# Kernel optimization log

Measured on AMD Instinct MI355X. Metric: run time of the kernel, lower is better.

The kernel has to match this reference:

```python
import jax, jax.numpy as jnp
import numpy as np

DIM = 128
LAYER_GNN = 3
LAYER_CNN = 3
WINDOW = 11
K = 2 * WINDOW + 1  # conv kernel size 23
N_FP = 100000
N_WORD = 10000
N_ATOMS = 8192
L_PROT = 8192


def setup_inputs() -> dict:
    key = jax.random.key(0)
    ks = jax.random.split(key, 12)
    s = 0.1
    # sparse binary molecular adjacency (avg degree ~16), math is still dense matmul
    adjacency = (jax.random.uniform(ks[2], (N_ATOMS, N_ATOMS)) < 0.002).astype(jnp.float32)
    return {
        "fingerprints": jax.random.randint(ks[0], (N_ATOMS,), 0, N_FP),
        "words": jax.random.randint(ks[1], (L_PROT,), 0, N_WORD),
        "adjacency": adjacency,
        "emb_fp": jax.random.normal(ks[3], (N_FP, DIM), jnp.float32) * s,
        "emb_word": jax.random.normal(ks[4], (N_WORD, DIM), jnp.float32) * s,
        "Wg": jax.random.normal(ks[5], (LAYER_GNN, DIM, DIM), jnp.float32) * s,
        "bg": jnp.zeros((LAYER_GNN, DIM), jnp.float32),
        "conv_w": jax.random.normal(ks[6], (LAYER_CNN, 1, 1, K, K), jnp.float32) * s,
        "conv_b": jnp.zeros((LAYER_CNN,), jnp.float32),
        "Wa": jax.random.normal(ks[7], (DIM, DIM), jnp.float32) * s,
        "ba": jnp.zeros((DIM,), jnp.float32),
        "Wo": jax.random.normal(ks[8], (2, 2 * DIM), jnp.float32) * s,
        "bo": jnp.zeros((2,), jnp.float32),
    }


def reference(fingerprints, words, adjacency, emb_fp, emb_word, Wg, bg,
              conv_w, conv_b, Wa, ba, Wo, bo):
    # ---- GNN over compound graph ----
    xs = emb_fp[fingerprints]                      # [N_ATOMS, DIM]
    for i in range(LAYER_GNN):
        hs = jax.nn.relu(xs @ Wg[i].T + bg[i])     # Linear + ReLU
        xs = xs + adjacency @ hs                   # adjacency message passing
    x_compound = jnp.sum(xs, axis=0, keepdims=True)  # [1, DIM]

    # ---- attention-CNN over protein words ----
    xs_p = emb_word[words]                         # [L_PROT, DIM]
    x = x_compound                                 # [1, DIM]
    for i in range(LAYER_CNN):
        img = xs_p[None, None]                     # [1,1,L,DIM]
        h = jax.lax.conv_general_dilated(
            img, conv_w[i], window_strides=(1, 1),
            padding=[(WINDOW, WINDOW), (WINDOW, WINDOW)],
            dimension_numbers=("NCHW", "OIHW", "NCHW"))
        hs = jax.nn.relu(h[0, 0] + conv_b[i])      # [L, DIM]
        x = jax.nn.relu(x @ Wa.T + ba)             # [1, DIM]
        hs = jax.nn.relu(hs @ Wa.T + ba)           # [L, DIM]
        weights = jnp.tanh(x @ hs.T)               # [1, L]
        xs_p = weights.T * hs                      # [L, DIM]
    x_protein = jnp.sum(xs_p, axis=0, keepdims=True)  # [1, DIM]

    y = jnp.concatenate([x_compound, x_protein], axis=1)  # [1, 2*DIM]
    z = jax.nn.softmax(y @ Wo.T + bo, axis=1)
    return z[0]  # [2]
```

## Files before the change

### kernel.cpp

```cpp
#include <hip/hip_runtime.h>
#include <hip/hip_cooperative_groups.h>
#include <math.h>

namespace cg = cooperative_groups;

#define DIM 128
#define NATOMS 8192
#define LPROT 8192
#define CAP 64
#define NF (NATOMS*DIM)
#define NB 256
#define RPB 32
#define TPB 1024


__device__ __forceinline__ void d_ell(int blk, int tid, const float* __restrict__ adj,
                                      int* __restrict__ ell, int* __restrict__ cnt) {
  int wv = tid >> 6, lane = tid & 63;
  for (int rr = 0; rr < 2; ++rr) {
    int row = blk * RPB + wv * 2 + rr;
    const float4* rp = (const float4*)(adj + (size_t)row * NATOMS);
    int* er = ell + (size_t)row * CAP;
    int c = 0;
    for (int it = 0; it < NATOMS / 256; ++it) {
      float4 v = rp[(size_t)it * 64 + lane];
      float f[4] = {v.x, v.y, v.z, v.w};
      #pragma unroll
      for (int j = 0; j < 4; ++j) {
        bool nz = (f[j] != 0.0f);
        unsigned long long m = __ballot(nz);
        if (nz) {
          int pos = c + __popcll(m & ((1ull << lane) - 1ull));
          if (pos < CAP) er[pos] = it * 256 + lane * 4 + j;
        }
        c += __popcll(m);
      }
    }
    if (lane == 0) cnt[row] = c > CAP ? CAP : c;
  }
}

__device__ __forceinline__ void d_stage_w(int tid, const float* __restrict__ WT, float* Ws) {
  for (int i = tid; i < 4096; i += TPB) {
    int r = i >> 5, c = i & 31;
    *(float4*)&Ws[r * 132 + c * 4] = *(const float4*)&WT[r * DIM + c * 4];
  }
}

__device__ __forceinline__ void d_stage_a(int tid, const float* __restrict__ A,
                                          size_t rbase, float* As) {
  for (int i = tid; i < 1024; i += TPB) {
    int r = i >> 5, c = i & 31;
    *(float4*)&As[r * 132 + c * 4] = *(const float4*)&A[(rbase + r) * DIM + c * 4];
  }
}

__device__ __forceinline__ void d_gemm44(int tid, const float* As, const float* Ws,
                                         const float* __restrict__ bias,
                                         float* out, int ostr, size_t obase) {
  if (tid < 256) {
    int j0 = (tid & 31) * 4, r0 = (tid >> 5) * 4;
    float acc[4][4];
    float4 b4 = *(const float4*)&bias[j0];
    #pragma unroll
    for (int ri = 0; ri < 4; ++ri) {
      acc[ri][0] = b4.x; acc[ri][1] = b4.y; acc[ri][2] = b4.z; acc[ri][3] = b4.w;
    }
    for (int k4 = 0; k4 < 32; ++k4) {
      float a[4][4], w[4][4];
      #pragma unroll
      for (int ri = 0; ri < 4; ++ri)
        *(float4*)a[ri] = *(const float4*)&As[(r0 + ri) * 132 + k4 * 4];
      #pragma unroll
      for (int kk = 0; kk < 4; ++kk)
        *(float4*)w[kk] = *(const float4*)&Ws[(k4 * 4 + kk) * 132 + j0];
      #pragma unroll
      for (int ri = 0; ri < 4; ++ri)
        #pragma unroll
        for (int kk = 0; kk < 4; ++kk) {
          acc[ri][0] += a[ri][kk] * w[kk][0];
          acc[ri][1] += a[ri][kk] * w[kk][1];
          acc[ri][2] += a[ri][kk] * w[kk][2];
          acc[ri][3] += a[ri][kk] * w[kk][3];
        }
    }
    #pragma unroll
    for (int ri = 0; ri < 4; ++ri) {
      float4 o;
      o.x = fmaxf(acc[ri][0], 0.f); o.y = fmaxf(acc[ri][1], 0.f);
      o.z = fmaxf(acc[ri][2], 0.f); o.w = fmaxf(acc[ri][3], 0.f);
      *(float4*)&out[(obase + r0 + ri) * (size_t)ostr + j0] = o;
    }
  }
}

__device__ __forceinline__ void d_spmv(int blk, int tid, const int* __restrict__ ell,
                                       const int* __restrict__ cnt,
                                       const float* __restrict__ hs, float* __restrict__ xs) {
  int wv = tid >> 6, lane = tid & 63;
  for (int rr = 0; rr < 2; ++rr) {
    size_t row = (size_t)blk * RPB + wv * 2 + rr;
    int n = cnt[row];
    const int* er = ell + row * CAP;
    float2 a2 = *(const float2*)&xs[row * DIM + lane * 2];
    int t = 0;
    for (; t + 4 <= n; t += 4) {
      int j0 = er[t], j1 = er[t + 1], j2 = er[t + 2], j3 = er[t + 3];
      float2 h0 = *(const float2*)&hs[(size_t)j0 * DIM + lane * 2];
      float2 h1 = *(const float2*)&hs[(size_t)j1 * DIM + lane * 2];
      float2 h2 = *(const float2*)&hs[(size_t)j2 * DIM + lane * 2];
      float2 h3 = *(const float2*)&hs[(size_t)j3 * DIM + lane * 2];
      a2.x += (h0.x + h1.x) + (h2.x + h3.x);
      a2.y += (h0.y + h1.y) + (h2.y + h3.y);
    }
    for (; t < n; ++t) {
      float2 h = *(const float2*)&hs[(size_t)er[t] * DIM + lane * 2];
      a2.x += h.x; a2.y += h.y;
    }
    *(float2*)&xs[row * DIM + lane * 2] = a2;
  }
}

__device__ __forceinline__ void d_colsum(int blk, int tid, const float* __restrict__ src,
                                         float* red, float* __restrict__ dst) {
  int c = tid & 127, h = tid >> 7;
  size_t rbase = (size_t)blk * RPB;
  float s = 0.f;
  for (int r = h; r < RPB; r += 8) s += src[(rbase + r) * DIM + c];
  red[h * DIM + c] = s;
  __syncthreads();
  if (h == 0) {
    float t2 = 0.f;
    #pragma unroll
    for (int w = 0; w < 8; ++w) t2 += red[w * DIM + c];
    atomicAdd(&dst[c], t2);
  }
}

__device__ __forceinline__ void d_xchain(int tid, const float* __restrict__ xc,
                                         const float* __restrict__ WaT,
                                         const float* __restrict__ ba,
                                         float* xb, float* __restrict__ xall) {
  if (tid < DIM) xb[tid] = xc[tid];
  __syncthreads();
  for (int i = 0; i < 3; ++i) {
    float a = 0.f;
    if (tid < DIM) {
      a = ba[tid];
      for (int k = 0; k < DIM; ++k) a += xb[k] * WaT[k * DIM + tid];
      a = fmaxf(a, 0.f);
    }
    __syncthreads();
    if (tid < DIM) { xb[tid] = a; xall[i * DIM + tid] = a; }
    __syncthreads();
  }
}

__device__ __forceinline__ void d_stage_tile(int blk, int tid, const float* __restrict__ cur,
                                             const float* __restrict__ cwl,
                                             float* U, float* wl) {
  for (int i = tid; i < 529; i += TPB) wl[i] = cwl[i];
  int l0 = blk * RPB;
  for (int i = tid; i < 54 * 156; i += TPB) {
    int ll = i / 156, dd = i % 156;
    int gl = l0 - 11 + ll, gd = dd - 11;
    float v = 0.f;
    if (gl >= 0 && gl < LPROT && (unsigned)gd < DIM)
      v = cur[(size_t)gl * DIM + gd];
    U[i] = v;
  }
}

__device__ __forceinline__ void d_conv(int tid, const float* U, const float* wl,
                                       float cbias, float* As) {
  int ro = tid >> 5, d0 = (tid & 31) * 4;
  float acc[4] = {0.f, 0.f, 0.f, 0.f};
  for (int a = 0; a < 23; ++a) {
    float r[26];
    #pragma unroll
    for (int q = 0; q < 6; ++q)
      *(float4*)&r[4 * q] = *(const float4*)&U[(ro + a) * 156 + d0 + 4 * q];
    r[24] = U[(ro + a) * 156 + d0 + 24];
    r[25] = U[(ro + a) * 156 + d0 + 25];
    #pragma unroll
    for (int b = 0; b < 23; ++b) {
      float wb = wl[a * 23 + b];
      #pragma unroll
      for (int m = 0; m < 4; ++m) acc[m] += r[b + m] * wb;
    }
  }
  #pragma unroll
  for (int m = 0; m < 4; ++m)
    As[ro * 132 + d0 + m] = fmaxf(acc[m] + cbias, 0.f);
}

__device__ __forceinline__ void d_attn(int blk, int tid, const float* hs2, const float* xrow,
                                       float* __restrict__ nxt, int last,
                                       float* red, float* __restrict__ xp) {
  int wv = tid >> 6, lane = tid & 63;
  size_t rbase = (size_t)blk * RPB;
  float x0 = xrow[lane * 2], x1 = xrow[lane * 2 + 1];
  float cx = 0.f, cy = 0.f;
  #pragma unroll
  for (int rr = 0; rr < 2; ++rr) {
    int row = wv * 2 + rr;
    float2 h = *(const float2*)&hs2[row * 132 + lane * 2];
    float p = h.x * x0 + h.y * x1;
    #pragma unroll
    for (int s = 32; s > 0; s >>= 1) p += __shfl_xor(p, s, 64);
    float wgt = tanhf(p);
    if (!last) {
      float2 o; o.x = wgt * h.x; o.y = wgt * h.y;
      *(float2*)&nxt[(rbase + row) * DIM + lane * 2] = o;
    } else { cx += wgt * h.x; cy += wgt * h.y; }
  }
  if (last) {
    red[wv * DIM + lane * 2] = cx;
    red[wv * DIM + lane * 2 + 1] = cy;
    __syncthreads();
    if (wv == 0) {
      float sx = 0.f, sy = 0.f;
      #pragma unroll
      for (int w = 0; w < 16; ++w) {
        sx += red[w * DIM + lane * 2];
        sy += red[w * DIM + lane * 2 + 1];
      }
      atomicAdd(&xp[lane * 2], sx);
      atomicAdd(&xp[lane * 2 + 1], sy);
    }
  }
}

__device__ __forceinline__ void d_final(int tid, const float* __restrict__ xc,
                                        const float* __restrict__ xp,
                                        const float* __restrict__ Wo,
                                        const float* __restrict__ bo,
                                        float* fs, float* __restrict__ out) {
  int wv = tid >> 6, lane = tid & 63;
  float p0 = 0.f, p1 = 0.f;
  if (tid < 256) {
    float y = (tid < DIM) ? xc[tid] : xp[tid - DIM];
    p0 = y * Wo[tid];
    p1 = y * Wo[256 + tid];
  }
  #pragma unroll
  for (int s = 32; s > 0; s >>= 1) { p0 += __shfl_xor(p0, s, 64); p1 += __shfl_xor(p1, s, 64); }
  if (tid < 256 && lane == 0) { fs[wv] = p0; fs[16 + wv] = p1; }
  __syncthreads();
  if (tid == 0) {
    float l0 = bo[0], l1 = bo[1];
    #pragma unroll
    for (int w = 0; w < 4; ++w) { l0 += fs[w]; l1 += fs[16 + w]; }
    float m = fmaxf(l0, l1);
    float e0 = expf(l0 - m), e1 = expf(l1 - m);
    out[0] = e0 / (e0 + e1);
    out[1] = e1 / (e0 + e1);
  }
}

__global__ __launch_bounds__(256) void k_prep(
    const int* __restrict__ fp, const int* __restrict__ words,
    const float* __restrict__ emb_fp, const float* __restrict__ emb_w,
    const float* __restrict__ Wg, const float* __restrict__ Wa,
    float* __restrict__ xs, float* __restrict__ xsp,
    float* __restrict__ WgT, float* __restrict__ WaT,
    float* __restrict__ xc, float* __restrict__ xp) {
  int b = blockIdx.x, tid = threadIdx.x;
  if (b < 1024) {
    int i = b * 256 + tid;
    int row = i >> 5, c4 = i & 31;
    ((float4*)(xs + (size_t)row * DIM))[c4] =
        ((const float4*)(emb_fp + (size_t)fp[row] * DIM))[c4];
  } else if (b < 2048) {
    int i = (b - 1024) * 256 + tid;
    int row = i >> 5, c4 = i & 31;
    ((float4*)(xsp + (size_t)row * DIM))[c4] =
        ((const float4*)(emb_w + (size_t)words[row] * DIM))[c4];
  } else if (b < 2112) {
    __shared__ float tile[32][33];
    int sub = b - 2048;
    int m = sub >> 4, t = sub & 15;
    int tx = t & 3, ty = t >> 2;
    const float* src = (m < 3) ? Wg + m * DIM * DIM : Wa;
    float*       dst = (m < 3) ? WgT + m * DIM * DIM : WaT;
    int x = tid & 31, y0 = tid >> 5;
    int xg = tx * 32 + x;
    for (int i = y0; i < 32; i += 8)
      tile[i][x] = src[(ty * 32 + i) * DIM + xg];
    __syncthreads();
    int xo = ty * 32 + x;
    for (int i = y0; i < 32; i += 8)
      dst[(tx * 32 + i) * DIM + xo] = tile[x][i];
  } else {
    if (tid < DIM) { xc[tid] = 0.f; xp[tid] = 0.f; }
  }
}

__global__ __launch_bounds__(TPB, 4) void kg(
    const float* __restrict__ adj, const float* __restrict__ WgT,
    const float* __restrict__ bg, const float* __restrict__ WaT,
    const float* __restrict__ ba, int* __restrict__ ell, int* __restrict__ cnt,
    float* __restrict__ xs, float* __restrict__ hsbA, float* __restrict__ hsbB,
    float* __restrict__ xc, float* __restrict__ xall) {
  cg::grid_group grid = cg::this_grid();
  __shared__ float Ws[128 * 132];
  __shared__ float As[32 * 132];
  __shared__ float red[8 * DIM];
  int tid = threadIdx.x, blk = blockIdx.x;
  size_t rbase = (size_t)blk * RPB;

  d_ell(blk, tid, adj, ell, cnt);
  __syncthreads();
  for (int layer = 0; layer < 3; ++layer) {
    float* hout = (layer == 1) ? hsbB : hsbA;
    d_stage_w(tid, WgT + (size_t)layer * DIM * DIM, Ws);
    d_stage_a(tid, xs, rbase, As);
    __syncthreads();
    d_gemm44(tid, As, Ws, bg + layer * DIM, hout, DIM, rbase);
    grid.sync();
    d_spmv(blk, tid, ell, cnt, hout, xs);
    __syncthreads();
  }
  d_colsum(blk, tid, xs, red, xc);
  grid.sync();
  if (blk == 0) d_xchain(tid, xc, WaT, ba, red, xall);
}

__global__ __launch_bounds__(TPB, 4) void kp(
    const float* __restrict__ cw, const float* __restrict__ cb,
    const float* __restrict__ WaT, const float* __restrict__ ba,
    const float* __restrict__ xall, const float* __restrict__ xc,
    const float* __restrict__ Wo, const float* __restrict__ bo,
    float* __restrict__ bufA, float* __restrict__ bufB,
    float* __restrict__ xp, float* __restrict__ out) {
  cg::grid_group grid = cg::this_grid();
  __shared__ float U[128 * 132];
  __shared__ float wl[529];
  __shared__ float As[32 * 132];
  __shared__ float hs2[32 * 132];
  __shared__ float xrow[DIM];
  __shared__ float fs[32];
  int tid = threadIdx.x, blk = blockIdx.x;

  const float* cur = bufA;
  float* nxt = bufB;
  for (int layer = 0; layer < 3; ++layer) {
    d_stage_tile(blk, tid, cur, cw + layer * 529, U, wl);
    if (tid < DIM) xrow[tid] = xall[layer * DIM + tid];
    __syncthreads();
    d_conv(tid, U, wl, cb[layer], As);
    __syncthreads();
    d_stage_w(tid, WaT, U);
    __syncthreads();
    d_gemm44(tid, As, U, ba, hs2, 132, 0);
    __syncthreads();
    d_attn(blk, tid, hs2, xrow, nxt, layer == 2, As, xp);
    grid.sync();
    const float* t = cur; cur = nxt; nxt = (float*)t;
  }
  if (blk == 0) d_final(tid, xc, xp, Wo, bo, fs, out);
}

__global__ __launch_bounds__(TPB, 4) void fb_ell(const float* __restrict__ adj,
                                                 int* __restrict__ ell, int* __restrict__ cnt) {
  d_ell(blockIdx.x, threadIdx.x, adj, ell, cnt);
}
__global__ __launch_bounds__(TPB, 4) void fb_ggemm(const float* __restrict__ WT,
                                                   const float* __restrict__ bias,
                                                   const float* __restrict__ xs,
                                                   float* __restrict__ hout) {
  __shared__ float Ws[128 * 132];
  __shared__ float As[32 * 132];
  int tid = threadIdx.x;
  size_t rbase = (size_t)blockIdx.x * RPB;
  d_stage_w(tid, WT, Ws);
  d_stage_a(tid, xs, rbase, As);
  __syncthreads();
  d_gemm44(tid, As, Ws, bias, hout, DIM, rbase);
}
__global__ __launch_bounds__(TPB, 4) void fb_spmv(const int* __restrict__ ell,
                                                  const int* __restrict__ cnt,
                                                  const float* __restrict__ hs,
                                                  float* __restrict__ xs) {
  d_spmv(blockIdx.x, threadIdx.x, ell, cnt, hs, xs);
}
__global__ __launch_bounds__(TPB, 4) void fb_colxc(const float* __restrict__ xs,
                                                   float* __restrict__ xc) {
  __shared__ float red[8 * DIM];
  d_colsum(blockIdx.x, threadIdx.x, xs, red, xc);
}
__global__ void fb_xchain(const float* __restrict__ xc, const float* __restrict__ WaT,
                          const float* __restrict__ ba, float* __restrict__ xall) {
  __shared__ float xb[DIM];
  d_xchain(threadIdx.x, xc, WaT, ba, xb, xall);
}
__global__ __launch_bounds__(TPB, 4) void fb_prot(const float* __restrict__ cur,
    float* __restrict__ nxt, const float* __restrict__ cwl, const float* __restrict__ cbp,
    const float* __restrict__ WaT, const float* __restrict__ ba,
    const float* __restrict__ xrow_g, float* __restrict__ xp, int last) {
  __shared__ float U[128 * 132];
  __shared__ float wl[529];
  __shared__ float As[32 * 132];
  __shared__ float hs2[32 * 132];
  __shared__ float xrow[DIM];
  int tid = threadIdx.x, blk = blockIdx.x;
  d_stage_tile(blk, tid, cur, cwl, U, wl);
  if (tid < DIM) xrow[tid] = xrow_g[tid];
  __syncthreads();
  d_conv(tid, U, wl, cbp[0], As);
  __syncthreads();
  d_stage_w(tid, WaT, U);
  __syncthreads();
  d_gemm44(tid, As, U, ba, hs2, 132, 0);
  __syncthreads();
  d_attn(blk, tid, hs2, xrow, nxt, last, As, xp);
}
__global__ void fb_final(const float* __restrict__ xc, const float* __restrict__ xp,
                         const float* __restrict__ Wo, const float* __restrict__ bo,
                         float* __restrict__ out) {
  __shared__ float fs[32];
  d_final(threadIdx.x, xc, xp, Wo, bo, fs, out);
}

extern "C" void kernel_launch(void* const* d_in, const int* in_sizes, int n_in,
                              void* d_out, int out_size, void* d_ws, size_t ws_size,
                              hipStream_t stream) {
  const int*   fp     = (const int*)d_in[0];
  const int*   words  = (const int*)d_in[1];
  const float* adj    = (const float*)d_in[2];
  const float* emb_fp = (const float*)d_in[3];
  const float* emb_w  = (const float*)d_in[4];
  const float* Wg     = (const float*)d_in[5];
  const float* bg     = (const float*)d_in[6];
  const float* cw     = (const float*)d_in[7];
  const float* cb     = (const float*)d_in[8];
  const float* Wa     = (const float*)d_in[9];
  const float* ba     = (const float*)d_in[10];
  const float* Wo     = (const float*)d_in[11];
  const float* bo     = (const float*)d_in[12];
  float* out = (float*)d_out;

  float* ws   = (float*)d_ws;
  float* xs   = ws;
  float* hsbA = ws + (size_t)NF;
  float* hsbB = ws + 2 * (size_t)NF;
  float* bufA = ws + 3 * (size_t)NF;
  int*   ell  = (int*)(ws + 4 * (size_t)NF);
  int*   cnt  = ell + (size_t)NATOMS * CAP;
  float* xc   = (float*)(cnt + NATOMS);
  float* xp   = xc + DIM;
  float* xall = xp + DIM;
  float* WgT  = xall + 3 * DIM;
  float* WaT  = WgT + 3 * DIM * DIM;
  float* bufB = hsbA;

  k_prep<<<dim3(2113), 256, 0, stream>>>(fp, words, emb_fp, emb_w, Wg, Wa,
                                         xs, bufA, WgT, WaT, xc, xp);

  int mg = 0, mp = 0;
  hipError_t e1 = hipOccupancyMaxActiveBlocksPerMultiprocessor(
      &mg, reinterpret_cast<const void*>(kg), TPB, 0);
  hipError_t e2 = hipOccupancyMaxActiveBlocksPerMultiprocessor(
      &mp, reinterpret_cast<const void*>(kp), TPB, 0);
  bool coop = (e1 == hipSuccess && e2 == hipSuccess && mg >= 1 && mp >= 1);

  if (coop) {
    void* ag[] = {(void*)&adj, (void*)&WgT, (void*)&bg, (void*)&WaT, (void*)&ba,
                  (void*)&ell, (void*)&cnt, (void*)&xs, (void*)&hsbA, (void*)&hsbB,
                  (void*)&xc, (void*)&xall};
    if (hipLaunchCooperativeKernel((void*)kg, dim3(NB), dim3(TPB), ag, 0, stream)
        != hipSuccess) {
      coop = false;
    } else {
      void* ap[] = {(void*)&cw, (void*)&cb, (void*)&WaT, (void*)&ba, (void*)&xall,
                    (void*)&xc, (void*)&Wo, (void*)&bo, (void*)&bufA, (void*)&bufB,
                    (void*)&xp, (void*)&out};
      if (hipLaunchCooperativeKernel((void*)kp, dim3(NB), dim3(TPB), ap, 0, stream)
          != hipSuccess)
        coop = false;
    }
  }

  if (!coop) {
    k_prep<<<dim3(2113), 256, 0, stream>>>(fp, words, emb_fp, emb_w, Wg, Wa,
                                           xs, bufA, WgT, WaT, xc, xp);
    fb_ell<<<dim3(NB), TPB, 0, stream>>>(adj, ell, cnt);
    for (int l = 0; l < 3; ++l) {
      float* ho = (l == 1) ? hsbB : hsbA;
      fb_ggemm<<<dim3(NB), TPB, 0, stream>>>(WgT + (size_t)l * DIM * DIM,
                                             bg + l * DIM, xs, ho);
      fb_spmv<<<dim3(NB), TPB, 0, stream>>>(ell, cnt, ho, xs);
    }
    fb_colxc<<<dim3(NB), TPB, 0, stream>>>(xs, xc);
    fb_xchain<<<dim3(1), 128, 0, stream>>>(xc, WaT, ba, xall);
    const float* cur = bufA; float* nxt = bufB;
    for (int l = 0; l < 3; ++l) {
      fb_prot<<<dim3(NB), TPB, 0, stream>>>(cur, nxt, cw + l * 529, cb + l, WaT, ba,
                                            xall + l * DIM, xp, l == 2 ? 1 : 0);
      const float* t = cur; cur = nxt; nxt = (float*)t;
    }
    fb_final<<<dim3(1), 256, 0, stream>>>(xc, xp, Wo, bo, out);
  }
}
```

Baseline: 290.2 us.

## Move ELL construction into prep kernel with prefetching and merge cooperative kernels

The adjacency-to-ELL scan moves out of the cooperative GNN kernel into the wide prep launch, with one wave per row and double-buffered float4 prefetches of eight loads at a time, so the 256MB adjacency read is spread across thousands of blocks instead of 256. The GNN and protein cooperative kernels are merged into one kernel with a grid sync between phases, removing a launch. The merged kernel's shared memory is the union of both kernels' arrays, which may reduce occupancy. The fallback path no longer re-runs prep or ELL building.

```diff
diff --git a/kernel.cpp b/kernel.cpp
--- a/kernel.cpp
+++ b/kernel.cpp
@@ -13,32 +13,6 @@
 #define RPB 32
 #define TPB 1024
 
-
-__device__ __forceinline__ void d_ell(int blk, int tid, const float* __restrict__ adj,
-                                      int* __restrict__ ell, int* __restrict__ cnt) {
-  int wv = tid >> 6, lane = tid & 63;
-  for (int rr = 0; rr < 2; ++rr) {
-    int row = blk * RPB + wv * 2 + rr;
-    const float4* rp = (const float4*)(adj + (size_t)row * NATOMS);
-    int* er = ell + (size_t)row * CAP;
-    int c = 0;
-    for (int it = 0; it < NATOMS / 256; ++it) {
-      float4 v = rp[(size_t)it * 64 + lane];
-      float f[4] = {v.x, v.y, v.z, v.w};
-      #pragma unroll
-      for (int j = 0; j < 4; ++j) {
-        bool nz = (f[j] != 0.0f);
-        unsigned long long m = __ballot(nz);
-        if (nz) {
-          int pos = c + __popcll(m & ((1ull << lane) - 1ull));
-          if (pos < CAP) er[pos] = it * 256 + lane * 4 + j;
-        }
-        c += __popcll(m);
-      }
-    }
-    if (lane == 0) cnt[row] = c > CAP ? CAP : c;
-  }
-}
 
 __device__ __forceinline__ void d_stage_w(int tid, const float* __restrict__ WT, float* Ws) {
   for (int i = tid; i < 4096; i += TPB) {
@@ -258,27 +232,62 @@
   }
 }
 
-__global__ __launch_bounds__(256) void k_prep(
+__global__ __launch_bounds__(256) void k_prep_build(
     const int* __restrict__ fp, const int* __restrict__ words,
     const float* __restrict__ emb_fp, const float* __restrict__ emb_w,
     const float* __restrict__ Wg, const float* __restrict__ Wa,
+    const float* __restrict__ adj,
     float* __restrict__ xs, float* __restrict__ xsp,
     float* __restrict__ WgT, float* __restrict__ WaT,
+    int* __restrict__ ell, int* __restrict__ cnt,
     float* __restrict__ xc, float* __restrict__ xp) {
   int b = blockIdx.x, tid = threadIdx.x;
-  if (b < 1024) {
-    int i = b * 256 + tid;
+  if (b < 2048) {
+    int wv = tid >> 6, lane = tid & 63;
+    int row = b * 4 + wv;
+    const float4* rp = (const float4*)(adj + (size_t)row * NATOMS);
+    int* er = ell + (size_t)row * CAP;
+    int c = 0;
+    float4 buf[8];
+    #pragma unroll
+    for (int u = 0; u < 8; ++u) buf[u] = rp[u * 64 + lane];
+    for (int it = 0; it < 32; it += 8) {
+      float4 nb[8];
+      if (it + 8 < 32) {
+        #pragma unroll
+        for (int u = 0; u < 8; ++u) nb[u] = rp[(it + 8 + u) * 64 + lane];
+      }
+      #pragma unroll
+      for (int u = 0; u < 8; ++u) {
+        float f[4] = {buf[u].x, buf[u].y, buf[u].z, buf[u].w};
+        #pragma unroll
+        for (int j = 0; j < 4; ++j) {
+          bool nz = (f[j] != 0.0f);
+          unsigned long long m = __ballot(nz);
+          if (nz) {
+            int pos = c + __popcll(m & ((1ull << lane) - 1ull));
+            if (pos < CAP) er[pos] = (it + u) * 256 + lane * 4 + j;
+          }
+          c += __popcll(m);
+        }
+      }
+      #pragma unroll
+      for (int u = 0; u < 8; ++u) buf[u] = nb[u];
+    }
+    if (lane == 0) cnt[row] = c > CAP ? CAP : c;
+  } else if (b < 3072) {
+    int i = (b - 2048) * 256 + tid;
     int row = i >> 5, c4 = i & 31;
     ((float4*)(xs + (size_t)row * DIM))[c4] =
         ((const float4*)(emb_fp + (size_t)fp[row] * DIM))[c4];
-  } else if (b < 2048) {
-    int i = (b - 1024) * 256 + tid;
+  } else if (b < 4096) {
+    int i = (b - 3072) * 256 + tid;
     int row = i >> 5, c4 = i & 31;
     ((float4*)(xsp + (size_t)row * DIM))[c4] =
         ((const float4*)(emb_w + (size_t)words[row] * DIM))[c4];
-  } else if (b < 2112) {
+  } else if (b < 4160) {
     __shared__ float tile[32][33];
-    int sub = b - 2048;
+    int sub = b - 4096;
     int m = sub >> 4, t = sub & 15;
     int tx = t & 3, ty = t >> 2;
     const float* src = (m < 3) ? Wg + m * DIM * DIM : Wa;
@@ -296,21 +305,27 @@
   }
 }
 
-__global__ __launch_bounds__(TPB, 4) void kg(
-    const float* __restrict__ adj, const float* __restrict__ WgT,
-    const float* __restrict__ bg, const float* __restrict__ WaT,
-    const float* __restrict__ ba, int* __restrict__ ell, int* __restrict__ cnt,
+__global__ __launch_bounds__(TPB, 4) void kmain(
+    const float* __restrict__ WgT, const float* __restrict__ bg,
+    const float* __restrict__ WaT, const float* __restrict__ ba,
+    const int* __restrict__ ell, const int* __restrict__ cnt,
+    const float* __restrict__ cw, const float* __restrict__ cb,
+    const float* __restrict__ Wo, const float* __restrict__ bo,
     float* __restrict__ xs, float* __restrict__ hsbA, float* __restrict__ hsbB,
-    float* __restrict__ xc, float* __restrict__ xall) {
+    float* __restrict__ bufA, float* __restrict__ bufB,
+    float* __restrict__ xc, float* __restrict__ xp,
+    float* __restrict__ xall, float* __restrict__ out) {
   cg::grid_group grid = cg::this_grid();
   __shared__ float Ws[128 * 132];
   __shared__ float As[32 * 132];
+  __shared__ float hs2[32 * 132];
   __shared__ float red[8 * DIM];
+  __shared__ float wl[529];
+  __shared__ float xrow[DIM];
+  __shared__ float fs[32];
   int tid = threadIdx.x, blk = blockIdx.x;
   size_t rbase = (size_t)blk * RPB;
 
-  d_ell(blk, tid, adj, ell, cnt);
-  __syncthreads();
   for (int layer = 0; layer < 3; ++layer) {
     float* hout = (layer == 1) ? hsbB : hsbA;
     d_stage_w(tid, WgT + (size_t)layer * DIM * DIM, Ws);
@@ -324,35 +339,19 @@
   d_colsum(blk, tid, xs, red, xc);
   grid.sync();
   if (blk == 0) d_xchain(tid, xc, WaT, ba, red, xall);
-}
-
-__global__ __launch_bounds__(TPB, 4) void kp(
-    const float* __restrict__ cw, const float* __restrict__ cb,
-    const float* __restrict__ WaT, const float* __restrict__ ba,
-    const float* __restrict__ xall, const float* __restrict__ xc,
-    const float* __restrict__ Wo, const float* __restrict__ bo,
-    float* __restrict__ bufA, float* __restrict__ bufB,
-    float* __restrict__ xp, float* __restrict__ out) {
-  cg::grid_group grid = cg::this_grid();
-  __shared__ float U[128 * 132];
-  __shared__ float wl[529];
-  __shared__ float As[32 * 132];
-  __shared__ float hs2[32 * 132];
-  __shared__ float xrow[DIM];
-  __shared__ float fs[32];
-  int tid = threadIdx.x, blk = blockIdx.x;
+  grid.sync();
 
   const float* cur = bufA;
   float* nxt = bufB;
   for (int layer = 0; layer < 3; ++layer) {
-    d_stage_tile(blk, tid, cur, cw + layer * 529, U, wl);
+    d_stage_tile(blk, tid, cur, cw + layer * 529, Ws, wl);
     if (tid < DIM) xrow[tid] = xall[layer * DIM + tid];
     __syncthreads();
-    d_conv(tid, U, wl, cb[layer], As);
-    __syncthreads();
-    d_stage_w(tid, WaT, U);
-    __syncthreads();
-    d_gemm44(tid, As, U, ba, hs2, 132, 0);
+    d_conv(tid, Ws, wl, cb[layer], As);
+    __syncthreads();
+    d_stage_w(tid, WaT, Ws);
+    __syncthreads();
+    d_gemm44(tid, As, Ws, ba, hs2, 132, 0);
     __syncthreads();
     d_attn(blk, tid, hs2, xrow, nxt, layer == 2, As, xp);
     grid.sync();
@@ -361,10 +360,6 @@
   if (blk == 0) d_final(tid, xc, xp, Wo, bo, fs, out);
 }
 
-__global__ __launch_bounds__(TPB, 4) void fb_ell(const float* __restrict__ adj,
-                                                 int* __restrict__ ell, int* __restrict__ cnt) {
-  d_ell(blockIdx.x, threadIdx.x, adj, ell, cnt);
-}
 __global__ __launch_bounds__(TPB, 4) void fb_ggemm(const float* __restrict__ WT,
                                                    const float* __restrict__ bias,
                                                    const float* __restrict__ xs,
@@ -454,37 +449,27 @@
   float* WaT  = WgT + 3 * DIM * DIM;
   float* bufB = hsbA;
 
-  k_prep<<<dim3(2113), 256, 0, stream>>>(fp, words, emb_fp, emb_w, Wg, Wa,
-                                         xs, bufA, WgT, WaT, xc, xp);
-
-  int mg = 0, mp = 0;
+  k_prep_build<<<dim3(4161), 256, 0, stream>>>(
+      fp, words, emb_fp, emb_w, Wg, Wa, adj,
+      xs, bufA, WgT, WaT, ell, cnt, xc, xp);
+
+  int mg = 0;
   hipError_t e1 = hipOccupancyMaxActiveBlocksPerMultiprocessor(
-      &mg, reinterpret_cast<const void*>(kg), TPB, 0);
-  hipError_t e2 = hipOccupancyMaxActiveBlocksPerMultiprocessor(
-      &mp, reinterpret_cast<const void*>(kp), TPB, 0);
-  bool coop = (e1 == hipSuccess && e2 == hipSuccess && mg >= 1 && mp >= 1);
+      &mg, reinterpret_cast<const void*>(kmain), TPB, 0);
+  bool coop = (e1 == hipSuccess && mg >= 1);
 
   if (coop) {
-    void* ag[] = {(void*)&adj, (void*)&WgT, (void*)&bg, (void*)&WaT, (void*)&ba,
-                  (void*)&ell, (void*)&cnt, (void*)&xs, (void*)&hsbA, (void*)&hsbB,
-                  (void*)&xc, (void*)&xall};
-    if (hipLaunchCooperativeKernel((void*)kg, dim3(NB), dim3(TPB), ag, 0, stream)
-        != hipSuccess) {
+    void* a[] = {(void*)&WgT, (void*)&bg, (void*)&WaT, (void*)&ba,
+                 (void*)&ell, (void*)&cnt, (void*)&cw, (void*)&cb,
+                 (void*)&Wo, (void*)&bo, (void*)&xs, (void*)&hsbA, (void*)&hsbB,
+                 (void*)&bufA, (void*)&bufB, (void*)&xc, (void*)&xp,
+                 (void*)&xall, (void*)&out};
+    if (hipLaunchCooperativeKernel((void*)kmain, dim3(NB), dim3(TPB), a, 0, stream)
+        != hipSuccess)
       coop = false;
-    } else {
-      void* ap[] = {(void*)&cw, (void*)&cb, (void*)&WaT, (void*)&ba, (void*)&xall,
-                    (void*)&xc, (void*)&Wo, (void*)&bo, (void*)&bufA, (void*)&bufB,
-                    (void*)&xp, (void*)&out};
-      if (hipLaunchCooperativeKernel((void*)kp, dim3(NB), dim3(TPB), ap, 0, stream)
-          != hipSuccess)
-        coop = false;
-    }
   }
 
   if (!coop) {
-    k_prep<<<dim3(2113), 256, 0, stream>>>(fp, words, emb_fp, emb_w, Wg, Wa,
-                                           xs, bufA, WgT, WaT, xc, xp);
-    fb_ell<<<dim3(NB), TPB, 0, stream>>>(adj, ell, cnt);
     for (int l = 0; l < 3; ++l) {
       float* ho = (l == 1) ? hsbB : hsbA;
       fb_ggemm<<<dim3(NB), TPB, 0, stream>>>(WgT + (size_t)l * DIM * DIM,
```

New measurement: 269.9 us. 7.0% less time.
